# Kernel tuning notes

Hardware: AMD Instinct MI355X
Metric: run time of the kernel (lower is better)

## Reference

```python
import jax, jax.numpy as jnp
import numpy as np


def setup_inputs() -> dict:
    key = jax.random.key(0)
    ks = jax.random.split(key, 12)
    B, S, IN, NBLK, DBLK = 64, 512, 512, 64, 16
    DHID = NBLK * DBLK
    sx = 1.0 / np.sqrt(IN)
    sh = 1.0 / np.sqrt(DHID)
    return {
        "x": jax.random.normal(ks[0], (B, S, IN), jnp.float32),
        "h0": jax.random.normal(ks[1], (1, DHID), jnp.float32) * 0.1,
        "c0": jax.random.normal(ks[2], (1, NBLK, DBLK), jnp.float32) * 0.1,
        "Wig": jax.random.normal(ks[3], (IN, NBLK), jnp.float32) * sx,
        "Uig": jax.random.normal(ks[4], (DHID, NBLK), jnp.float32) * sh,
        "big": jax.random.normal(ks[5], (NBLK,), jnp.float32) * sx,
        "Wog": jax.random.normal(ks[6], (IN, NBLK), jnp.float32) * sx,
        "Uog": jax.random.normal(ks[7], (DHID, NBLK), jnp.float32) * sh,
        "bog": jax.random.normal(ks[8], (NBLK,), jnp.float32) * sx,
        "Wmc": jax.random.normal(ks[9], (IN, DHID), jnp.float32) * sx,
        "Umc": jax.random.normal(ks[10], (DHID, DHID), jnp.float32) * sh,
        "bmc": jax.random.normal(ks[11], (DHID,), jnp.float32) * sx,
    }


def reference(x, h0, c0, Wig, Uig, big, Wog, Uog, bog, Wmc, Umc, bmc):
    B, S, _ = x.shape
    n_blk, d_blk = c0.shape[1], c0.shape[2]
    # Precompute input projections for all timesteps (time-major for scan).
    xig = (x @ Wig + big).swapaxes(0, 1)  # (S, B, n_blk)
    xog = (x @ Wog + bog).swapaxes(0, 1)  # (S, B, n_blk)
    xmc = (x @ Wmc + bmc).swapaxes(0, 1)  # (S, B, d_hid)

    h_init = jnp.broadcast_to(h0, (B, h0.shape[1]))           # (B, d_hid)
    c_init = jnp.broadcast_to(c0, (B, n_blk, d_blk))           # (B, n_blk, d_blk)

    def step(carry, inp):
        h, c = carry
        xig_t, xog_t, xmc_t = inp
        ig = jax.nn.sigmoid(xig_t + h @ Uig)                   # (B, n_blk)
        og = jax.nn.sigmoid(xog_t + h @ Uog)                   # (B, n_blk)
        g = jnp.tanh(xmc_t + h @ Umc).reshape(B, n_blk, d_blk)
        c_new = c + ig[:, :, None] * g                         # CEC update (no forget gate)
        h_new = (og[:, :, None] * jnp.tanh(c_new)).reshape(B, n_blk * d_blk)
        return (h_new, c_new), (h_new, c_new)

    _, (h_seq, c_seq) = jax.lax.scan(step, (h_init, c_init), (xig, xog, xmc))
    return h_seq.swapaxes(0, 1), c_seq.swapaxes(0, 1)  # (B,S,d_hid), (B,S,n_blk,d_blk)
```

## Files before the change

kernel.cpp:

```cpp
#include <hip/hip_runtime.h>

using short8 = __attribute__((ext_vector_type(8))) short;
using sh4    = __attribute__((ext_vector_type(4))) short;
using f32x4  = __attribute__((ext_vector_type(4))) float;

#define DEVI static __device__ __forceinline__

DEVI unsigned short f2bf(float f) {
  union { float f; unsigned u; } v; v.f = f;
  unsigned r = v.u + 0x7FFFu + ((v.u >> 16) & 1u);
  return (unsigned short)(r >> 16);
}
DEVI float bf2f(unsigned short h) {
  union { unsigned u; float f; } v; v.u = (unsigned)h << 16;
  return v.f;
}
DEVI void splitf(float f, unsigned short& hi, unsigned short& lo) {
  unsigned short h = f2bf(f);
  hi = h;
  lo = f2bf(f - bf2f(h));
}

static constexpr int  B_  = 64;
static constexpr int  S_  = 512;
static constexpr int  IN_ = 512;
static constexpr int  NB_ = 64;
static constexpr int  DH_ = 1024;
static constexpr long M_  = (long)B_ * S_;

__global__ void prep_kernel(const float* __restrict__ Wmc, const float* __restrict__ Wig,
                            const float* __restrict__ Wog,
                            const float* __restrict__ Umc, const float* __restrict__ Uig,
                            const float* __restrict__ Uog,
                            const float* __restrict__ h0,
                            unsigned short* __restrict__ WmcTh, unsigned short* __restrict__ WmcTl,
                            unsigned short* __restrict__ WigTh, unsigned short* __restrict__ WigTl,
                            unsigned short* __restrict__ WogTh, unsigned short* __restrict__ WogTl,
                            unsigned short* __restrict__ UmcTh, unsigned short* __restrict__ UmcTl,
                            unsigned short* __restrict__ UigTh, unsigned short* __restrict__ UigTl,
                            unsigned short* __restrict__ UogTh, unsigned short* __restrict__ UogTl,
                            unsigned short* __restrict__ hbh,   unsigned short* __restrict__ hbl)
{
  const long e0 = 1024L * 512;
  const long e1 = e0 + 64L * 512;
  const long e2 = e1 + 64L * 512;
  const long e3 = e2 + 1024L * 1024;
  const long e4 = e3 + 64L * 1024;
  const long e5 = e4 + 64L * 1024;
  const long e6 = e5 + 64L * 1024;
  for (long i = (long)blockIdx.x * blockDim.x + threadIdx.x; i < e6;
       i += (long)gridDim.x * blockDim.x) {
    float v; unsigned short *ph, *pl; long idx;
    if (i < e0) {
      idx = i; long n = idx >> 9, k = idx & 511;
      v = Wmc[k * 1024 + n]; ph = WmcTh; pl = WmcTl;
    } else if (i < e1) {
      idx = i - e0; long n = idx >> 9, k = idx & 511;
      v = Wig[k * 64 + n]; ph = WigTh; pl = WigTl;
    } else if (i < e2) {
      idx = i - e1; long n = idx >> 9, k = idx & 511;
      v = Wog[k * 64 + n]; ph = WogTh; pl = WogTl;
    } else if (i < e3) {
      idx = i - e2; long n = idx >> 10, k = idx & 1023;
      v = Umc[k * 1024 + n]; ph = UmcTh; pl = UmcTl;
    } else if (i < e4) {
      idx = i - e3; long n = idx >> 10, k = idx & 1023;
      v = Uig[k * 64 + n]; ph = UigTh; pl = UigTl;
    } else if (i < e5) {
      idx = i - e4; long n = idx >> 10, k = idx & 1023;
      v = Uog[k * 64 + n]; ph = UogTh; pl = UogTl;
    } else {
      idx = i - e5;
      v = h0[idx & 1023]; ph = hbh; pl = hbl;
    }
    unsigned short hi, lo; splitf(v, hi, lo);
    ph[idx] = hi; pl[idx] = lo;
  }
}

__global__ __launch_bounds__(256) void gemm_split(
    const float* __restrict__ A,
    const unsigned short* __restrict__ BTh,
    const unsigned short* __restrict__ BTl,
    const float* __restrict__ bias,
    float* __restrict__ C,
    int N)
{
  const int K = 512;
  __shared__ unsigned short Ah[128][72];
  __shared__ unsigned short Alo[128][72];
  __shared__ unsigned short Bh[64][72];
  __shared__ unsigned short Blo[64][72];
  int tid = threadIdx.x, lane = tid & 63, w = tid >> 6;
  int wm = w & 1, wn = w >> 1;
  int m0 = blockIdx.x * 128, n0 = blockIdx.y * 64;
  f32x4 acc[4][2] = {};
  for (int kt = 0; kt < K; kt += 64) {
    __syncthreads();
#pragma unroll
    for (int i = 0; i < 8; ++i) {
      int c = tid + i * 256; int r = c >> 4, o = (c & 15) * 4;
      float4 v = *(const float4*)&A[(long)(m0 + r) * K + kt + o];
      sh4 hi, lo;
      { unsigned short h_, l_;
        splitf(v.x, h_, l_); hi[0] = (short)h_; lo[0] = (short)l_;
        splitf(v.y, h_, l_); hi[1] = (short)h_; lo[1] = (short)l_;
        splitf(v.z, h_, l_); hi[2] = (short)h_; lo[2] = (short)l_;
        splitf(v.w, h_, l_); hi[3] = (short)h_; lo[3] = (short)l_; }
      *(sh4*)&Ah[r][o]  = hi;
      *(sh4*)&Alo[r][o] = lo;
    }
#pragma unroll
    for (int i = 0; i < 2; ++i) {
      int c = tid + i * 256; int r = c >> 3, o = (c & 7) * 8;
      *(short8*)&Bh[r][o]  = *(const short8*)&BTh[(long)(n0 + r) * K + kt + o];
      *(short8*)&Blo[r][o] = *(const short8*)&BTl[(long)(n0 + r) * K + kt + o];
    }
    __syncthreads();
#pragma unroll
    for (int ks = 0; ks < 2; ++ks) {
      short8 ah[4], al[4], bh[2], bl[2];
      int kk = ks * 32 + (lane >> 4) * 8;
#pragma unroll
      for (int mt = 0; mt < 4; ++mt) {
        ah[mt] = *(const short8*)&Ah[wm * 64 + mt * 16 + (lane & 15)][kk];
        al[mt] = *(const short8*)&Alo[wm * 64 + mt * 16 + (lane & 15)][kk];
      }
#pragma unroll
      for (int nt = 0; nt < 2; ++nt) {
        bh[nt] = *(const short8*)&Bh[wn * 32 + nt * 16 + (lane & 15)][kk];
        bl[nt] = *(const short8*)&Blo[wn * 32 + nt * 16 + (lane & 15)][kk];
      }
#pragma unroll
      for (int mt = 0; mt < 4; ++mt)
#pragma unroll
        for (int nt = 0; nt < 2; ++nt) {
          acc[mt][nt] = __builtin_amdgcn_mfma_f32_16x16x32_bf16(
              ah[mt], bl[nt], acc[mt][nt], 0, 0, 0);
          acc[mt][nt] = __builtin_amdgcn_mfma_f32_16x16x32_bf16(
              al[mt], bh[nt], acc[mt][nt], 0, 0, 0);
          acc[mt][nt] = __builtin_amdgcn_mfma_f32_16x16x32_bf16(
              ah[mt], bh[nt], acc[mt][nt], 0, 0, 0);
        }
    }
  }
#pragma unroll
  for (int mt = 0; mt < 4; ++mt)
#pragma unroll
    for (int nt = 0; nt < 2; ++nt) {
      int col = n0 + wn * 32 + nt * 16 + (lane & 15);
      float bv = bias[col];
#pragma unroll
      for (int r = 0; r < 4; ++r) {
        int row = m0 + wm * 64 + mt * 16 + (lane >> 4) * 4 + r;
        C[(long)row * N + col] = acc[mt][nt][r] + bv;
      }
    }
}

__global__ __launch_bounds__(256) void lstm_step(
    const unsigned short* __restrict__ hih, const unsigned short* __restrict__ hil,
    unsigned short* __restrict__ hoh,       unsigned short* __restrict__ hol,
    const unsigned short* __restrict__ UmcTh, const unsigned short* __restrict__ UmcTl,
    const unsigned short* __restrict__ UigTh, const unsigned short* __restrict__ UigTl,
    const unsigned short* __restrict__ UogTh, const unsigned short* __restrict__ UogTl,
    const float* __restrict__ xig,
    const float* __restrict__ xog,
    const float* __restrict__ c0,
    float* __restrict__ hseq,
    float* __restrict__ cseq,
    int t)
{
  int tid = threadIdx.x, lane = tid & 63, w = tid >> 6;
  int blk = blockIdx.x, mg = blockIdx.y;
  __shared__ float pA[4][16][16];
  __shared__ float pG[4][16][16];
  f32x4 acc0 = {}, acc1 = {};
  bool isog = ((lane & 15) == 1);
  const unsigned short* g_h = (isog ? UogTh : UigTh) + (long)blk * DH_;
  const unsigned short* g_l = (isog ? UogTl : UigTl) + (long)blk * DH_;
  long arow = (long)(mg * 16 + (lane & 15)) * DH_;
  long brow = (long)(blk * 16 + (lane & 15)) * DH_;
#pragma unroll
  for (int k8 = 0; k8 < 8; ++k8) {
    int kk = w * 256 + k8 * 32 + (lane >> 4) * 8;
    short8 ah = *(const short8*)&hih[arow + kk];
    short8 al = *(const short8*)&hil[arow + kk];
    short8 b0h = *(const short8*)&UmcTh[brow + kk];
    short8 b0l = *(const short8*)&UmcTl[brow + kk];
    short8 b1h = *(const short8*)&g_h[kk];
    short8 b1l = *(const short8*)&g_l[kk];
    acc0 = __builtin_amdgcn_mfma_f32_16x16x32_bf16(ah, b0l, acc0, 0, 0, 0);
    acc0 = __builtin_amdgcn_mfma_f32_16x16x32_bf16(al, b0h, acc0, 0, 0, 0);
    acc0 = __builtin_amdgcn_mfma_f32_16x16x32_bf16(ah, b0h, acc0, 0, 0, 0);
    acc1 = __builtin_amdgcn_mfma_f32_16x16x32_bf16(ah, b1l, acc1, 0, 0, 0);
    acc1 = __builtin_amdgcn_mfma_f32_16x16x32_bf16(al, b1h, acc1, 0, 0, 0);
    acc1 = __builtin_amdgcn_mfma_f32_16x16x32_bf16(ah, b1h, acc1, 0, 0, 0);
  }
#pragma unroll
  for (int r = 0; r < 4; ++r) {
    pA[w][(lane >> 4) * 4 + r][lane & 15] = acc0[r];
    pG[w][(lane >> 4) * 4 + r][lane & 15] = acc1[r];
  }
  __syncthreads();
  int bi = tid >> 4, ji = tid & 15;
  int b = mg * 16 + bi, j = blk * 16 + ji;
  float gsum = pA[0][bi][ji] + pA[1][bi][ji] + pA[2][bi][ji] + pA[3][bi][ji];
  float isum = pG[0][bi][0] + pG[1][bi][0] + pG[2][bi][0] + pG[3][bi][0];
  float osum = pG[0][bi][1] + pG[1][bi][1] + pG[2][bi][1] + pG[3][bi][1];
  long base = ((long)b * S_ + t) * DH_ + j;
  float gpre = hseq[base] + gsum;
  float ipre = xig[((long)b * S_ + t) * NB_ + blk] + isum;
  float opre = xog[((long)b * S_ + t) * NB_ + blk] + osum;
  float ig = 1.f / (1.f + __expf(-ipre));
  float og = 1.f / (1.f + __expf(-opre));
  float g  = tanhf(gpre);
  float cprev = (t == 0) ? c0[j] : cseq[base - DH_];
  float cn = cprev + ig * g;
  float hv = og * tanhf(cn);
  cseq[base] = cn;
  hseq[base] = hv;
  long ho = (long)b * DH_ + j;
  unsigned short hh, hl; splitf(hv, hh, hl);
  hoh[ho] = hh; hol[ho] = hl;
}

extern "C" void kernel_launch(void* const* d_in, const int* in_sizes, int n_in,
                              void* d_out, int out_size, void* d_ws, size_t ws_size,
                              hipStream_t stream) {
  const float* x   = (const float*)d_in[0];
  const float* h0  = (const float*)d_in[1];
  const float* c0  = (const float*)d_in[2];
  const float* Wig = (const float*)d_in[3];
  const float* Uig = (const float*)d_in[4];
  const float* big = (const float*)d_in[5];
  const float* Wog = (const float*)d_in[6];
  const float* Uog = (const float*)d_in[7];
  const float* bog = (const float*)d_in[8];
  const float* Wmc = (const float*)d_in[9];
  const float* Umc = (const float*)d_in[10];
  const float* bmc = (const float*)d_in[11];

  char* ws = (char*)d_ws;
  size_t off = 0;
  auto alloc = [&](size_t bytes) { void* p = ws + off; off += (bytes + 255) & ~255UL; return p; };
  unsigned short* WmcTh = (unsigned short*)alloc(1024L * 512 * 2);
  unsigned short* WmcTl = (unsigned short*)alloc(1024L * 512 * 2);
  unsigned short* WigTh = (unsigned short*)alloc(64L * 512 * 2);
  unsigned short* WigTl = (unsigned short*)alloc(64L * 512 * 2);
  unsigned short* WogTh = (unsigned short*)alloc(64L * 512 * 2);
  unsigned short* WogTl = (unsigned short*)alloc(64L * 512 * 2);
  unsigned short* UmcTh = (unsigned short*)alloc(1024L * 1024 * 2);
  unsigned short* UmcTl = (unsigned short*)alloc(1024L * 1024 * 2);
  unsigned short* UigTh = (unsigned short*)alloc(64L * 1024 * 2);
  unsigned short* UigTl = (unsigned short*)alloc(64L * 1024 * 2);
  unsigned short* UogTh = (unsigned short*)alloc(64L * 1024 * 2);
  unsigned short* UogTl = (unsigned short*)alloc(64L * 1024 * 2);
  unsigned short* hAh   = (unsigned short*)alloc(64L * 1024 * 2);
  unsigned short* hAl   = (unsigned short*)alloc(64L * 1024 * 2);
  unsigned short* hBh   = (unsigned short*)alloc(64L * 1024 * 2);
  unsigned short* hBl   = (unsigned short*)alloc(64L * 1024 * 2);
  float* xig            = (float*)alloc(M_ * 64 * 4);
  float* xog            = (float*)alloc(M_ * 64 * 4);

  float* hseq = (float*)d_out;
  float* cseq = hseq + M_ * DH_;

  prep_kernel<<<2048, 256, 0, stream>>>(Wmc, Wig, Wog, Umc, Uig, Uog, h0,
                                        WmcTh, WmcTl, WigTh, WigTl, WogTh, WogTl,
                                        UmcTh, UmcTl, UigTh, UigTl, UogTh, UogTl,
                                        hAh, hAl);
  gemm_split<<<dim3(256, 16), 256, 0, stream>>>(x, WmcTh, WmcTl, bmc, hseq, 1024);
  gemm_split<<<dim3(256, 1), 256, 0, stream>>>(x, WigTh, WigTl, big, xig, 64);
  gemm_split<<<dim3(256, 1), 256, 0, stream>>>(x, WogTh, WogTl, bog, xog, 64);

  for (int t = 0; t < S_; ++t) {
    const unsigned short* hih = (t & 1) ? hBh : hAh;
    const unsigned short* hil = (t & 1) ? hBl : hAl;
    unsigned short* hoh       = (t & 1) ? hAh : hBh;
    unsigned short* hol       = (t & 1) ? hAl : hBl;
    lstm_step<<<dim3(64, 4), 256, 0, stream>>>(hih, hil, hoh, hol,
                                               UmcTh, UmcTl, UigTh, UigTl,
                                               UogTh, UogTl, xig, xog, c0,
                                               hseq, cseq, t);
  }
}
```

Measured before the change: 4.426 ms.

## Replace per-timestep launches with persistent scan kernel using flag-based grid sync

The 512 separate step launches become one persistent kernel with 32 blocks. Each block keeps its slice of the recurrent weights and the cell state in registers across all timesteps. Blocks synchronise per step through device-scope atomic flags that prep_kernel zeroes. This is meant to remove launch overhead and repeated weight loads. The cost is heavy register pressure, spin-wait latency, and reliance on all 32 blocks being co-resident.

```diff
diff --git a/kernel.cpp b/kernel.cpp
--- a/kernel.cpp
+++ b/kernel.cpp
@@ -27,6 +27,8 @@
 static constexpr int  NB_ = 64;
 static constexpr int  DH_ = 1024;
 static constexpr long M_  = (long)B_ * S_;
+
+#define MFMA16(a, b, c) __builtin_amdgcn_mfma_f32_16x16x32_bf16(a, b, c, 0, 0, 0)
 
 __global__ void prep_kernel(const float* __restrict__ Wmc, const float* __restrict__ Wig,
                             const float* __restrict__ Wog,
@@ -39,7 +41,8 @@
                             unsigned short* __restrict__ UmcTh, unsigned short* __restrict__ UmcTl,
                             unsigned short* __restrict__ UigTh, unsigned short* __restrict__ UigTl,
                             unsigned short* __restrict__ UogTh, unsigned short* __restrict__ UogTl,
-                            unsigned short* __restrict__ hbh,   unsigned short* __restrict__ hbl)
+                            unsigned short* __restrict__ hbh,   unsigned short* __restrict__ hbl,
+                            int* __restrict__ flags)
 {
   const long e0 = 1024L * 512;
   const long e1 = e0 + 64L * 512;
@@ -48,8 +51,10 @@
   const long e4 = e3 + 64L * 1024;
   const long e5 = e4 + 64L * 1024;
   const long e6 = e5 + 64L * 1024;
-  for (long i = (long)blockIdx.x * blockDim.x + threadIdx.x; i < e6;
+  const long e7 = e6 + 512L * 32;
+  for (long i = (long)blockIdx.x * blockDim.x + threadIdx.x; i < e7;
        i += (long)gridDim.x * blockDim.x) {
+    if (i >= e6) { flags[i - e6] = 0; continue; }
     float v; unsigned short *ph, *pl; long idx;
     if (i < e0) {
       idx = i; long n = idx >> 9, k = idx & 511;
@@ -135,12 +140,9 @@
       for (int mt = 0; mt < 4; ++mt)
 #pragma unroll
         for (int nt = 0; nt < 2; ++nt) {
-          acc[mt][nt] = __builtin_amdgcn_mfma_f32_16x16x32_bf16(
-              ah[mt], bl[nt], acc[mt][nt], 0, 0, 0);
-          acc[mt][nt] = __builtin_amdgcn_mfma_f32_16x16x32_bf16(
-              al[mt], bh[nt], acc[mt][nt], 0, 0, 0);
-          acc[mt][nt] = __builtin_amdgcn_mfma_f32_16x16x32_bf16(
-              ah[mt], bh[nt], acc[mt][nt], 0, 0, 0);
+          acc[mt][nt] = MFMA16(ah[mt], bl[nt], acc[mt][nt]);
+          acc[mt][nt] = MFMA16(al[mt], bh[nt], acc[mt][nt]);
+          acc[mt][nt] = MFMA16(ah[mt], bh[nt], acc[mt][nt]);
         }
     }
   }
@@ -158,71 +160,141 @@
     }
 }
 
-__global__ __launch_bounds__(256) void lstm_step(
-    const unsigned short* __restrict__ hih, const unsigned short* __restrict__ hil,
-    unsigned short* __restrict__ hoh,       unsigned short* __restrict__ hol,
+__global__ __launch_bounds__(256, 1) void lstm_scan(
+    unsigned short* __restrict__ hAh, unsigned short* __restrict__ hAl,
+    unsigned short* __restrict__ hBh, unsigned short* __restrict__ hBl,
     const unsigned short* __restrict__ UmcTh, const unsigned short* __restrict__ UmcTl,
     const unsigned short* __restrict__ UigTh, const unsigned short* __restrict__ UigTl,
     const unsigned short* __restrict__ UogTh, const unsigned short* __restrict__ UogTl,
-    const float* __restrict__ xig,
-    const float* __restrict__ xog,
+    const float* __restrict__ xig, const float* __restrict__ xog,
     const float* __restrict__ c0,
-    float* __restrict__ hseq,
-    float* __restrict__ cseq,
-    int t)
+    float* __restrict__ hseq, float* __restrict__ cseq,
+    int* __restrict__ flags)
 {
-  int tid = threadIdx.x, lane = tid & 63, w = tid >> 6;
-  int blk = blockIdx.x, mg = blockIdx.y;
-  __shared__ float pA[4][16][16];
-  __shared__ float pG[4][16][16];
-  f32x4 acc0 = {}, acc1 = {};
-  bool isog = ((lane & 15) == 1);
-  const unsigned short* g_h = (isog ? UogTh : UigTh) + (long)blk * DH_;
-  const unsigned short* g_l = (isog ? UogTl : UigTl) + (long)blk * DH_;
-  long arow = (long)(mg * 16 + (lane & 15)) * DH_;
-  long brow = (long)(blk * 16 + (lane & 15)) * DH_;
-#pragma unroll
-  for (int k8 = 0; k8 < 8; ++k8) {
-    int kk = w * 256 + k8 * 32 + (lane >> 4) * 8;
-    short8 ah = *(const short8*)&hih[arow + kk];
-    short8 al = *(const short8*)&hil[arow + kk];
-    short8 b0h = *(const short8*)&UmcTh[brow + kk];
-    short8 b0l = *(const short8*)&UmcTl[brow + kk];
-    short8 b1h = *(const short8*)&g_h[kk];
-    short8 b1l = *(const short8*)&g_l[kk];
-    acc0 = __builtin_amdgcn_mfma_f32_16x16x32_bf16(ah, b0l, acc0, 0, 0, 0);
-    acc0 = __builtin_amdgcn_mfma_f32_16x16x32_bf16(al, b0h, acc0, 0, 0, 0);
-    acc0 = __builtin_amdgcn_mfma_f32_16x16x32_bf16(ah, b0h, acc0, 0, 0, 0);
-    acc1 = __builtin_amdgcn_mfma_f32_16x16x32_bf16(ah, b1l, acc1, 0, 0, 0);
-    acc1 = __builtin_amdgcn_mfma_f32_16x16x32_bf16(al, b1h, acc1, 0, 0, 0);
-    acc1 = __builtin_amdgcn_mfma_f32_16x16x32_bf16(ah, b1h, acc1, 0, 0, 0);
-  }
-#pragma unroll
-  for (int r = 0; r < 4; ++r) {
-    pA[w][(lane >> 4) * 4 + r][lane & 15] = acc0[r];
-    pG[w][(lane >> 4) * 4 + r][lane & 15] = acc1[r];
-  }
-  __syncthreads();
-  int bi = tid >> 4, ji = tid & 15;
-  int b = mg * 16 + bi, j = blk * 16 + ji;
-  float gsum = pA[0][bi][ji] + pA[1][bi][ji] + pA[2][bi][ji] + pA[3][bi][ji];
-  float isum = pG[0][bi][0] + pG[1][bi][0] + pG[2][bi][0] + pG[3][bi][0];
-  float osum = pG[0][bi][1] + pG[1][bi][1] + pG[2][bi][1] + pG[3][bi][1];
-  long base = ((long)b * S_ + t) * DH_ + j;
-  float gpre = hseq[base] + gsum;
-  float ipre = xig[((long)b * S_ + t) * NB_ + blk] + isum;
-  float opre = xog[((long)b * S_ + t) * NB_ + blk] + osum;
-  float ig = 1.f / (1.f + __expf(-ipre));
-  float og = 1.f / (1.f + __expf(-opre));
-  float g  = tanhf(gpre);
-  float cprev = (t == 0) ? c0[j] : cseq[base - DH_];
-  float cn = cprev + ig * g;
-  float hv = og * tanhf(cn);
-  cseq[base] = cn;
-  hseq[base] = hv;
-  long ho = (long)b * DH_ + j;
-  unsigned short hh, hl; splitf(hv, hh, hl);
-  hoh[ho] = hh; hol[ho] = hl;
+  __shared__ float pA[4][64][33];
+  __shared__ float pG[4][64][17];
+  const int tid = threadIdx.x, lane = tid & 63, w = tid >> 6;
+  const int n = blockIdx.x;
+
+  short8 b0h[2][8], b0l[2][8], b1h[8], b1l[8];
+  {
+    int c = lane & 15;
+    int s = c & 1, dl = (c >> 1) & 1;
+    const unsigned short *gh, *gl;
+    if (c < 4) {
+      gh = (s ? UogTh : UigTh) + (long)(2 * n + dl) * DH_;
+      gl = (s ? UogTl : UigTl) + (long)(2 * n + dl) * DH_;
+    } else {
+      gh = UigTh + (long)(2 * n) * DH_;
+      gl = UigTl + (long)(2 * n) * DH_;
+    }
+#pragma unroll
+    for (int k8 = 0; k8 < 8; ++k8) {
+      int kk = w * 256 + k8 * 32 + (lane >> 4) * 8;
+#pragma unroll
+      for (int nt = 0; nt < 2; ++nt) {
+        long br = (long)(32 * n + 16 * nt + c) * DH_ + kk;
+        b0h[nt][k8] = *(const short8*)&UmcTh[br];
+        b0l[nt][k8] = *(const short8*)&UmcTl[br];
+      }
+      b1h[k8] = *(const short8*)&gh[kk];
+      b1l[k8] = *(const short8*)&gl[kk];
+    }
+  }
+  float c_reg[8];
+  {
+    float cv = c0[32 * n + (tid & 31)];
+#pragma unroll
+    for (int e = 0; e < 8; ++e) c_reg[e] = cv;
+  }
+
+  for (int t = 0; t < S_; ++t) {
+    unsigned short *hh, *hl, *oh, *ol;
+    if (t & 1) { hh = hBh; hl = hBl; oh = hAh; ol = hAl; }
+    else       { hh = hAh; hl = hAl; oh = hBh; ol = hBl; }
+
+    if (t) {
+      if (lane < 32) {
+        const int* f = flags + (t - 1) * 32;
+        long guard = 0;
+        while (__hip_atomic_load(&f[lane], __ATOMIC_RELAXED,
+                                 __HIP_MEMORY_SCOPE_AGENT) == 0 &&
+               guard < 20000000L) {
+          __builtin_amdgcn_s_sleep(2);
+          ++guard;
+        }
+      }
+      __threadfence();
+    }
+
+    f32x4 acc0[2][4] = {};
+    f32x4 acc1[4] = {};
+#pragma unroll
+    for (int k8 = 0; k8 < 8; ++k8) {
+      int kk = w * 256 + k8 * 32 + (lane >> 4) * 8;
+      short8 ah[4], al[4];
+#pragma unroll
+      for (int mt = 0; mt < 4; ++mt) {
+        long ar = (long)(mt * 16 + (lane & 15)) * DH_ + kk;
+        ah[mt] = *(const short8*)&hh[ar];
+        al[mt] = *(const short8*)&hl[ar];
+      }
+#pragma unroll
+      for (int mt = 0; mt < 4; ++mt) {
+#pragma unroll
+        for (int nt = 0; nt < 2; ++nt) {
+          acc0[nt][mt] = MFMA16(ah[mt], b0l[nt][k8], acc0[nt][mt]);
+          acc0[nt][mt] = MFMA16(al[mt], b0h[nt][k8], acc0[nt][mt]);
+          acc0[nt][mt] = MFMA16(ah[mt], b0h[nt][k8], acc0[nt][mt]);
+        }
+        acc1[mt] = MFMA16(ah[mt], b1l[k8], acc1[mt]);
+        acc1[mt] = MFMA16(al[mt], b1h[k8], acc1[mt]);
+        acc1[mt] = MFMA16(ah[mt], b1h[k8], acc1[mt]);
+      }
+    }
+#pragma unroll
+    for (int mt = 0; mt < 4; ++mt) {
+#pragma unroll
+      for (int r = 0; r < 4; ++r) {
+        int row = mt * 16 + (lane >> 4) * 4 + r;
+#pragma unroll
+        for (int nt = 0; nt < 2; ++nt)
+          pA[w][row][nt * 16 + (lane & 15)] = acc0[nt][mt][r];
+        pG[w][row][lane & 15] = acc1[mt][r];
+      }
+    }
+    __syncthreads();
+#pragma unroll
+    for (int e = 0; e < 8; ++e) {
+      int idx = tid + e * 256;
+      int bi = idx >> 5, jl = idx & 31, bl = jl >> 4;
+      float gsum = pA[0][bi][jl] + pA[1][bi][jl] + pA[2][bi][jl] + pA[3][bi][jl];
+      float isum = pG[0][bi][2*bl]   + pG[1][bi][2*bl]   + pG[2][bi][2*bl]   + pG[3][bi][2*bl];
+      float osum = pG[0][bi][2*bl+1] + pG[1][bi][2*bl+1] + pG[2][bi][2*bl+1] + pG[3][bi][2*bl+1];
+      int j = 32 * n + jl;
+      long base = ((long)bi * S_ + t) * DH_ + j;
+      long xb   = ((long)bi * S_ + t) * NB_ + 2 * n + bl;
+      float gpre = hseq[base] + gsum;
+      float ipre = xig[xb] + isum;
+      float opre = xog[xb] + osum;
+      float ig = 1.f / (1.f + __expf(-ipre));
+      float og = 1.f / (1.f + __expf(-opre));
+      float g  = tanhf(gpre);
+      float cn = c_reg[e] + ig * g;
+      float hv = og * tanhf(cn);
+      c_reg[e] = cn;
+      cseq[base] = cn;
+      hseq[base] = hv;
+      unsigned short hhv, hlv; splitf(hv, hhv, hlv);
+      long ho = (long)bi * DH_ + j;
+      oh[ho] = hhv; ol[ho] = hlv;
+    }
+    __threadfence();
+    __syncthreads();
+    if (tid == 0)
+      __hip_atomic_store(&flags[t * 32 + n], 1, __ATOMIC_RELEASE,
+                         __HIP_MEMORY_SCOPE_AGENT);
+  }
 }
 
 extern "C" void kernel_launch(void* const* d_in, const int* in_sizes, int n_in,
@@ -262,6 +334,7 @@
   unsigned short* hBl   = (unsigned short*)alloc(64L * 1024 * 2);
   float* xig            = (float*)alloc(M_ * 64 * 4);
   float* xog            = (float*)alloc(M_ * 64 * 4);
+  int*   flags          = (int*)alloc(512L * 32 * 4);
 
   float* hseq = (float*)d_out;
   float* cseq = hseq + M_ * DH_;
@@ -269,19 +342,12 @@
   prep_kernel<<<2048, 256, 0, stream>>>(Wmc, Wig, Wog, Umc, Uig, Uog, h0,
                                         WmcTh, WmcTl, WigTh, WigTl, WogTh, WogTl,
                                         UmcTh, UmcTl, UigTh, UigTl, UogTh, UogTl,
-                                        hAh, hAl);
+                                        hAh, hAl, flags);
   gemm_split<<<dim3(256, 16), 256, 0, stream>>>(x, WmcTh, WmcTl, bmc, hseq, 1024);
   gemm_split<<<dim3(256, 1), 256, 0, stream>>>(x, WigTh, WigTl, big, xig, 64);
   gemm_split<<<dim3(256, 1), 256, 0, stream>>>(x, WogTh, WogTl, bog, xog, 64);
 
-  for (int t = 0; t < S_; ++t) {
-    const unsigned short* hih = (t & 1) ? hBh : hAh;
-    const unsigned short* hil = (t & 1) ? hBl : hAl;
-    unsigned short* hoh       = (t & 1) ? hAh : hBh;
-    unsigned short* hol       = (t & 1) ? hAl : hBl;
-    lstm_step<<<dim3(64, 4), 256, 0, stream>>>(hih, hil, hoh, hol,
-                                               UmcTh, UmcTl, UigTh, UigTl,
-                                               UogTh, UogTl, xig, xog, c0,
-                                               hseq, cseq, t);
-  }
-}
+  lstm_scan<<<32, 256, 0, stream>>>(hAh, hAl, hBh, hBl,
+                                    UmcTh, UmcTl, UigTh, UigTl, UogTh, UogTl,
+                                    xig, xog, c0, hseq, cseq, flags);
+}
```

New measurement: 11.96 ms. 2.7x slower.
